# Kernel optimization log

Measured on AMD Instinct MI355X. Metric: run time of the kernel, lower is better.

## Reference

```python
import jax, jax.numpy as jnp
import numpy as np

N = 16384      # total nodes in batched graph
B = 64         # number of graphs (dgl.batch)
DEG = 8        # random in-degree (self-loops added on top)
C = 128        # feature width
H = 2          # heads in middle blocks
EH = 8         # E: heads of attn_seq / codebook entries
DEPTH = 2
IN = 8         # max_node_color (one-hot input width)
NE = N * DEG + N  # edges incl. self-loops


def layernorm(x, g, b, eps=1e-5):
    mu = jnp.mean(x, axis=-1, keepdims=True)
    var = jnp.mean(jnp.square(x - mu), axis=-1, keepdims=True)
    return (x - mu) * jax.lax.rsqrt(var + eps) * g + b


def gatv2(x, src, dst, Ws, bs, Wd, bd, attn):
    # DGL GATv2Conv (eval mode, attn_drop inactive, share_weights=False)
    h, c = attn.shape
    n = x.shape[0]
    el = (x @ Ws + bs).reshape(n, h, c)   # fc_src
    er = (x @ Wd + bd).reshape(n, h, c)   # fc_dst
    e = jax.nn.leaky_relu(el[src] + er[dst], negative_slope=0.2)  # [E,h,c]
    logits = jnp.einsum('ehc,hc->eh', e, attn)                    # [E,h]
    # edge softmax over incoming edges of each dst node
    m = jax.ops.segment_max(logits, dst, num_segments=n)
    a = jnp.exp(logits - m[dst])
    z = jax.ops.segment_sum(a, dst, num_segments=n)
    a = a / z[dst]
    return jax.ops.segment_sum(el[src] * a[..., None], dst, num_segments=n)  # [n,h,c]


def setup_inputs() -> dict:
    key = jax.random.key(0)
    ks = iter(jax.random.split(key, 64))
    nrm = lambda *s: jax.random.normal(next(ks), s, jnp.float32) * 0.05
    colors = jax.random.randint(next(ks), (N,), 0, IN)
    feats = jax.nn.one_hot(colors, IN, dtype=jnp.float32)
    loops = jnp.arange(N)
    src = jnp.concatenate([jax.random.randint(next(ks), (N * DEG,), 0, N), loops])
    dst = jnp.concatenate([jax.random.randint(next(ks), (N * DEG,), 0, N), loops])
    graph_ids = jnp.arange(N) // (N // B)
    inp = dict(feats=feats, src=src, dst=dst, graph_ids=graph_ids)
    # attn_up: GATv2Conv(IN -> C, 1 head)
    inp.update(up_Ws=nrm(IN, C), up_bs=nrm(C), up_Wd=nrm(IN, C), up_bd=nrm(C), up_attn=nrm(1, C))
    # depth blocks: GATv2Conv(C -> C, H heads) + ff
    inp.update(L_Ws=nrm(DEPTH, C, H * C), L_bs=nrm(DEPTH, H * C),
               L_Wd=nrm(DEPTH, C, H * C), L_bd=nrm(DEPTH, H * C),
               L_attn=nrm(DEPTH, H, C),
               ff_ln_g=jnp.ones((DEPTH, C), jnp.float32), ff_ln_b=jnp.zeros((DEPTH, C), jnp.float32),
               ff_W1=nrm(DEPTH, C, 2 * C), ff_b1=nrm(DEPTH, 2 * C),
               ff_W2=nrm(DEPTH, 2 * C, C), ff_b2=nrm(DEPTH, C),
               ff_W3=nrm(DEPTH, H * C, C), ff_b3=nrm(DEPTH, C))
    # attn_seq: GATv2Conv(C -> C, EH heads) + ff_seq
    inp.update(seq_Ws=nrm(C, EH * C), seq_bs=nrm(EH * C),
               seq_Wd=nrm(C, EH * C), seq_bd=nrm(EH * C),
               seq_attn=nrm(EH, C),
               fs_ln_g=jnp.ones((C,), jnp.float32), fs_ln_b=jnp.zeros((C,), jnp.float32),
               fs_W1=nrm(C, 2 * C), fs_b1=nrm(2 * C),
               fs_W2=nrm(2 * C, C), fs_b2=nrm(C),
               gate_W=nrm(EH * C, 1), gate_b=nrm(1))
    return inp


def reference(feats, src, dst, graph_ids,
              up_Ws, up_bs, up_Wd, up_bd, up_attn,
              L_Ws, L_bs, L_Wd, L_bd, L_attn,
              ff_ln_g, ff_ln_b, ff_W1, ff_b1, ff_W2, ff_b2, ff_W3, ff_b3,
              seq_Ws, seq_bs, seq_Wd, seq_bd, seq_attn,
              fs_ln_g, fs_ln_b, fs_W1, fs_b1, fs_W2, fs_b2,
              gate_W, gate_b):
    # attn_up (1 head) -> flatten to [N, C]
    x = gatv2(feats, src, dst, up_Ws, up_bs, up_Wd, up_bd, up_attn).reshape(N, C)
    for l in range(DEPTH):
        h = gatv2(x, src, dst, L_Ws[l], L_bs[l], L_Wd[l], L_bd[l], L_attn[l])  # [N,H,C]
        h = layernorm(h, ff_ln_g[l], ff_ln_b[l])
        h = jax.nn.gelu(h @ ff_W1[l] + ff_b1[l], approximate=False)
        h = h @ ff_W2[l] + ff_b2[l]                              # [N,H,C]
        x = h.reshape(N, H * C) @ ff_W3[l] + ff_b3[l]            # [N,C]
    y = gatv2(x, src, dst, seq_Ws, seq_bs, seq_Wd, seq_bd, seq_attn)  # [N,EH,C]
    y = layernorm(y, fs_ln_g, fs_ln_b)
    y = jax.nn.gelu(y @ fs_W1 + fs_b1, approximate=False) @ fs_W2 + fs_b2
    y = y.reshape(N, EH * C)
    # GlobalAttentionPooling: softmax(gate) over nodes within each graph
    gate = y @ gate_W + gate_b                                   # [N,1]
    gm = jax.ops.segment_max(gate, graph_ids, num_segments=B)
    ga = jnp.exp(gate - gm[graph_ids])
    gz = jax.ops.segment_sum(ga, graph_ids, num_segments=B)
    ga = ga / gz[graph_ids]
    pooled = jax.ops.segment_sum(ga * y, graph_ids, num_segments=B)  # [B, EH*C]
    return jnp.tanh(pooled.reshape(B, EH, C))
```

## Files before the change

kernel.cpp:

```cpp
#include <hip/hip_runtime.h>
#include <hip/hip_bf16.h>

typedef __hip_bfloat16 bf16;
typedef __attribute__((ext_vector_type(8))) short short8;
typedef __attribute__((ext_vector_type(4))) float f32x4;

#define NN 16384
#define NB 64
#define NE_TOT (NN*8 + NN)
#define CW 128

__device__ __forceinline__ float b2f(bf16 x){ return __bfloat162float(x); }
__device__ __forceinline__ bf16  f2b(float x){ return __float2bfloat16(x); }
__device__ __forceinline__ float lrelu(float x){ return fmaxf(x, 0.2f*x); }
__device__ __forceinline__ float gelu_f(float x){ return 0.5f*x*(1.f + erff(x*0.70710678118654752f)); }
__device__ __forceinline__ float us2f(unsigned int u){ return __uint_as_float(u << 16); }
__device__ __forceinline__ unsigned short f2us(float x){ return __builtin_bit_cast(unsigned short, f2b(x)); }

__device__ __forceinline__ void async16(const void* g, void* l){
  __builtin_amdgcn_global_load_lds((const __attribute__((address_space(1))) void*)g,
                                   (__attribute__((address_space(3))) void*)l, 16, 0, 0);
}

__global__ void k_detect(const unsigned short* __restrict__ f, int* __restrict__ flag){
  __shared__ int cnt;
  if(threadIdx.x == 0) cnt = 0;
  __syncthreads();
  int c = 0;
  for(int i = threadIdx.x; i < 2048; i += 256)
    if(f[2*i] == 0x3F80) c++;
  atomicAdd(&cnt, c);
  __syncthreads();
  if(threadIdx.x == 0) *flag = (cnt > 0) ? 0 : 1;
}

struct ConvArgs { const void* in[32]; bf16* out[32]; int n[32]; int tk[32]; int tj[32]; int ls[32]; };
__global__ __launch_bounds__(256) void k_conv_all(ConvArgs a, const int* __restrict__ flag){
  int which = blockIdx.y;
  int t = blockIdx.x*256 + threadIdx.x;
  int n = a.n[which];
  if(t >= n) return;
  float v = (*flag) ? ((const float*)a.in[which])[t] : b2f(((const bf16*)a.in[which])[t]);
  int tj = a.tj[which];
  if(tj == 0){ a.out[which][t] = f2b(v); return; }
  int tk = a.tk[which], kj = tk*tj;
  int l = t / kj, r = t - l*kj;
  int k = r / tj, j = r - k*tj;
  a.out[which][l*a.ls[which] + j*tk + k] = f2b(v);
}

__global__ void k_zero2(int* __restrict__ a, int* __restrict__ b, int n){
  int i = blockIdx.x*blockDim.x + threadIdx.x;
  if(i < n){ a[i] = 0; b[i] = 0; }
}
__global__ void k_hist(const int* __restrict__ dst, int* __restrict__ deg, int ne){
  int e = blockIdx.x*blockDim.x + threadIdx.x;
  if(e < ne) atomicAdd(&deg[dst[e]], 1);
}
__global__ void k_scan(const int* __restrict__ deg, int* __restrict__ off){
  __shared__ int s[256];
  int t = threadIdx.x;
  const int chunk = NN/256;
  int base = t*chunk;
  int sum = 0;
  for(int i=0;i<chunk;i++) sum += deg[base+i];
  s[t] = sum; __syncthreads();
  for(int o=1;o<256;o<<=1){
    int v = (t >= o) ? s[t-o] : 0;
    __syncthreads();
    s[t] += v;
    __syncthreads();
  }
  int run = (t == 0) ? 0 : s[t-1];
  for(int i=0;i<chunk;i++){ off[base+i] = run; run += deg[base+i]; }
  if(t == 255) off[NN] = run;
}
__global__ void k_scatter(const int* __restrict__ src, const int* __restrict__ dst,
                          const int* __restrict__ off, int* __restrict__ cursor,
                          int* __restrict__ csr_src, int ne){
  int e = blockIdx.x*blockDim.x + threadIdx.x;
  if(e < ne){
    int d = dst[e];
    int p = off[d] + atomicAdd(&cursor[d], 1);
    csr_src[p] = src[e];
  }
}

__global__ __launch_bounds__(128) void k_up(const bf16* __restrict__ feats,
    const bf16* __restrict__ Ws, const bf16* __restrict__ bs,
    const bf16* __restrict__ Wd, const bf16* __restrict__ bd,
    bf16* __restrict__ eler){
  int n = blockIdx.x, c = threadIdx.x;
  __shared__ float f[8];
  if(c < 8) f[c] = b2f(feats[n*8 + c]);
  __syncthreads();
  float a = b2f(bs[c]), b = b2f(bd[c]);
  #pragma unroll
  for(int k=0;k<8;k++){
    float fv = f[k];
    a += fv*b2f(Ws[k*CW + c]);
    b += fv*b2f(Wd[k*CW + c]);
  }
  eler[(size_t)n*256 + c]       = f2b(a);
  eler[(size_t)n*256 + 128 + c] = f2b(b);
}

template<int ACT>
__global__ __launch_bounds__(256) void k_mm(
    const bf16* __restrict__ A, int gshA, int gstrA,
    const bf16* __restrict__ WT, const bf16* __restrict__ bias,
    bf16* __restrict__ C, int gshC, int gstrC,
    int K, int J){
  __shared__ char smem[32768];
  short* As = (short*)smem;
  short* Bs = (short*)(smem + 16384);
  int tid = threadIdx.x, w = tid >> 6, lane = tid & 63;
  int l15 = lane & 15, q = lane >> 4;
  int wm = w >> 1, wn = w & 1;
  int bm = blockIdx.y*128, bn = blockIdx.x*128;

  f32x4 acc[4][4];
  #pragma unroll
  for(int i=0;i<4;i++)
    #pragma unroll
    for(int j=0;j<4;j++) acc[i][j] = (f32x4)0.f;

  int srow = w*32 + (lane >> 2);
  int scol = (lane & 3)*8;
  const bf16* gA[2]; const bf16* gB[2];
  short* lA[2]; short* lB[2];
  int mskA = (1 << gshA) - 1;
  #pragma unroll
  for(int a=0;a<2;a++){
    int rowA = bm + srow + a*16;
    gA[a] = A  + (size_t)(rowA >> gshA)*(size_t)gstrA + (size_t)(rowA & mskA)*K + scol;
    gB[a] = WT + (size_t)(bn + srow + a*16)*K + scol;
    lA[a] = As + (w*32 + a*16)*32;
    lB[a] = Bs + (w*32 + a*16)*32;
  }

  for(int kt=0; kt<K; kt+=64){
    #pragma unroll
    for(int a=0;a<2;a++)
      #pragma unroll
      for(int kh=0;kh<2;kh++){
        async16(gA[a] + kt + kh*32, lA[a] + kh*4096);
        async16(gB[a] + kt + kh*32, lB[a] + kh*4096);
      }
    __syncthreads();
    #pragma unroll
    for(int kh=0;kh<2;kh++){
      short8 af[4], bfr[4];
      #pragma unroll
      for(int i=0;i<4;i++) af[i]  = *(short8*)&As[kh*4096 + (wm*64 + i*16 + l15)*32 + q*8];
      #pragma unroll
      for(int j=0;j<4;j++) bfr[j] = *(short8*)&Bs[kh*4096 + (wn*64 + j*16 + l15)*32 + q*8];
      #pragma unroll
      for(int i=0;i<4;i++)
        #pragma unroll
        for(int j=0;j<4;j++)
          acc[i][j] = __builtin_amdgcn_mfma_f32_16x16x32_bf16(af[i], bfr[j], acc[i][j], 0, 0, 0);
    }
    __syncthreads();
  }

  float* ep = (float*)(smem + w*4352);
  int rr = lane >> 2;
  int cc = (lane & 3)*16;
  int mskC = (1 << gshC) - 1;
  #pragma unroll
  for(int i=0;i<4;i++){
    #pragma unroll
    for(int j=0;j<4;j++){
      float bv = b2f(bias[bn + wn*64 + j*16 + l15]);
      #pragma unroll
      for(int r=0;r<4;r++){
        float v = acc[i][j][r] + bv;
        if(ACT == 1) v = gelu_f(v);
        ep[(q*4+r)*68 + j*16 + l15] = v;
      }
    }
    float4 v0 = *(float4*)&ep[rr*68 + cc];
    float4 v1 = *(float4*)&ep[rr*68 + cc + 4];
    float4 v2 = *(float4*)&ep[rr*68 + cc + 8];
    float4 v3 = *(float4*)&ep[rr*68 + cc + 12];
    float vv[16] = {v0.x,v0.y,v0.z,v0.w, v1.x,v1.y,v1.z,v1.w,
                    v2.x,v2.y,v2.z,v2.w, v3.x,v3.y,v3.z,v3.w};
    unsigned int u[8];
    #pragma unroll
    for(int k=0;k<8;k++)
      u[k] = (unsigned int)f2us(vv[2*k]) | ((unsigned int)f2us(vv[2*k+1]) << 16);
    int row = bm + wm*64 + i*16 + rr;
    bf16* cp = C + (size_t)(row >> gshC)*(size_t)gstrC + (size_t)(row & mskC)*J + bn + wn*64 + cc;
    *(uint4*)cp       = make_uint4(u[0],u[1],u[2],u[3]);
    *(uint4*)(cp + 8) = make_uint4(u[4],u[5],u[6],u[7]);
  }
}

__global__ __launch_bounds__(256) void k_ff(
    const bf16* __restrict__ A, int gshA, int gstrA,
    const bf16* __restrict__ W1T, const bf16* __restrict__ b1,
    const bf16* __restrict__ W2T, const bf16* __restrict__ b2,
    bf16* __restrict__ C, int gshC, int gstrC){
  __shared__ short Wb[8704];
  __shared__ short Hs[8320];
  int tid = threadIdx.x, w = tid >> 6, lane = tid & 63;
  int l15 = lane & 15, q = lane >> 4;
  int bm = blockIdx.x*32;
  int mskA = (1 << gshA) - 1, mskC = (1 << gshC) - 1;
  int mt = w & 1, jg = w >> 1;

  int rowA = bm + mt*16 + l15;
  const bf16* ap = A + (size_t)(rowA >> gshA)*(size_t)gstrA + (size_t)(rowA & mskA)*128;
  short8 af[4];
  #pragma unroll
  for(int ki=0;ki<4;ki++) af[ki] = *(const short8*)&ap[ki*32 + q*8];

  for(int jt=0; jt<4; jt++){
    #pragma unroll
    for(int it=0;it<4;it++){
      int slot = tid + it*256;
      int r = slot >> 4, c8 = slot & 15;
      *(int4*)&Wb[r*132 + c8*8] = *(const int4*)&W1T[(size_t)(jt*64 + r)*128 + c8*8];
    }
    __syncthreads();
    f32x4 acc1[2] = {(f32x4)0.f, (f32x4)0.f};
    #pragma unroll
    for(int ki=0;ki<4;ki++){
      #pragma unroll
      for(int t=0;t<2;t++){
        int jrow = (jg*2 + t)*16 + l15;
        short8 bfr = *(short8*)&Wb[jrow*132 + ki*32 + q*8];
        acc1[t] = __builtin_amdgcn_mfma_f32_16x16x32_bf16(af[ki], bfr, acc1[t], 0, 0, 0);
      }
    }
    #pragma unroll
    for(int t=0;t<2;t++){
      int jcol = jt*64 + (jg*2 + t)*16 + l15;
      float bv = b2f(b1[jcol]);
      #pragma unroll
      for(int r=0;r<4;r++){
        float v = gelu_f(acc1[t][r] + bv);
        Hs[(mt*16 + q*4 + r)*260 + jcol] = (short)f2us(v);
      }
    }
    __syncthreads();
  }

  f32x4 acc2[4];
  #pragma unroll
  for(int t=0;t<4;t++) acc2[t] = (f32x4)0.f;
  for(int kc=0; kc<4; kc++){
    #pragma unroll
    for(int it=0;it<4;it++){
      int slot = tid + it*256;
      int r = slot >> 3, c8 = slot & 7;
      *(int4*)&Wb[r*68 + c8*8] = *(const int4*)&W2T[(size_t)r*256 + kc*64 + c8*8];
    }
    __syncthreads();
    #pragma unroll
    for(int ki=0;ki<2;ki++){
      short8 haf = *(short8*)&Hs[(mt*16 + l15)*260 + kc*64 + ki*32 + q*8];
      #pragma unroll
      for(int t=0;t<4;t++){
        int jrow = (jg*4 + t)*16 + l15;
        short8 bfr = *(short8*)&Wb[jrow*68 + ki*32 + q*8];
        acc2[t] = __builtin_amdgcn_mfma_f32_16x16x32_bf16(haf, bfr, acc2[t], 0, 0, 0);
      }
    }
    __syncthreads();
  }

  float* epf = (float*)Hs;
  #pragma unroll
  for(int t=0;t<4;t++){
    int jcol = (jg*4 + t)*16 + l15;
    float bv = b2f(b2[jcol]);
    #pragma unroll
    for(int r=0;r<4;r++)
      epf[(mt*16 + q*4 + r)*130 + jcol] = acc2[t][r] + bv;
  }
  __syncthreads();
  int row = tid >> 3, cseg = (tid & 7)*16;
  float4 v0 = *(float4*)&epf[row*130 + cseg];
  float4 v1 = *(float4*)&epf[row*130 + cseg + 4];
  float4 v2 = *(float4*)&epf[row*130 + cseg + 8];
  float4 v3 = *(float4*)&epf[row*130 + cseg + 12];
  float vv[16] = {v0.x,v0.y,v0.z,v0.w, v1.x,v1.y,v1.z,v1.w,
                  v2.x,v2.y,v2.z,v2.w, v3.x,v3.y,v3.z,v3.w};
  unsigned int u[8];
  #pragma unroll
  for(int k=0;k<8;k++)
    u[k] = (unsigned int)f2us(vv[2*k]) | ((unsigned int)f2us(vv[2*k+1]) << 16);
  int rowC = bm + row;
  bf16* cpb = C + (size_t)(rowC >> gshC)*(size_t)gstrC + (size_t)(rowC & mskC)*128 + cseg;
  *(uint4*)cpb       = make_uint4(u[0],u[1],u[2],u[3]);
  *(uint4*)(cpb + 8) = make_uint4(u[4],u[5],u[6],u[7]);
}

template<int E>
__device__ __forceinline__ void load_row(const bf16* p, float* f){
  if constexpr (E == 2){
    unsigned int v = *(const unsigned int*)p;
    f[0] = us2f(v & 0xffffu); f[1] = __uint_as_float(v & 0xffff0000u);
  } else if constexpr (E == 4){
    uint2 v = *(const uint2*)p;
    f[0] = us2f(v.x & 0xffffu); f[1] = __uint_as_float(v.x & 0xffff0000u);
    f[2] = us2f(v.y & 0xffffu); f[3] = __uint_as_float(v.y & 0xffff0000u);
  } else if constexpr (E == 8){
    uint4 a = *(const uint4*)p;
    unsigned int vs[4] = {a.x,a.y,a.z,a.w};
    #pragma unroll
    for(int i=0;i<4;i++){
      f[2*i]   = us2f(vs[i] & 0xffffu);
      f[2*i+1] = __uint_as_float(vs[i] & 0xffff0000u);
    }
  } else {
    uint4 a = *(const uint4*)p;
    uint4 b = *(const uint4*)(p + 8);
    unsigned int vs[8] = {a.x,a.y,a.z,a.w,b.x,b.y,b.z,b.w};
    #pragma unroll
    for(int i=0;i<8;i++){
      f[2*i]   = us2f(vs[i] & 0xffffu);
      f[2*i+1] = __uint_as_float(vs[i] & 0xffff0000u);
    }
  }
}
template<int E>
__device__ __forceinline__ void store_row(bf16* p, const float* f){
  unsigned int vs[E/2];
  #pragma unroll
  for(int i=0;i<E/2;i++)
    vs[i] = (unsigned int)f2us(f[2*i]) | ((unsigned int)f2us(f[2*i+1]) << 16);
  if constexpr (E == 2){ *(unsigned int*)p = vs[0]; }
  else if constexpr (E == 4){ *(uint2*)p = make_uint2(vs[0], vs[1]); }
  else if constexpr (E == 8){ *(uint4*)p = make_uint4(vs[0], vs[1], vs[2], vs[3]); }
  else {
    *(uint4*)p       = make_uint4(vs[0], vs[1], vs[2], vs[3]);
    *(uint4*)(p + 8) = make_uint4(vs[4], vs[5], vs[6], vs[7]);
  }
}

template<int H, bool LNF, int SSH>
__global__ __launch_bounds__(256) void k_gat(const int* __restrict__ off, const int* __restrict__ csr_src,
    const bf16* __restrict__ el, const bf16* __restrict__ er, const bf16* __restrict__ attn,
    const bf16* __restrict__ lng, const bf16* __restrict__ lnb, bf16* __restrict__ out,
    int rsn_in, int rsh_in, int rsn_out, int rsh_out){
  constexpr int EPL = 2*H;
  constexpr int G   = 64/H;
  int w = threadIdx.x >> 6, lane = threadIdx.x & 63;
  int nv = blockIdx.x*4 + w;
  int node = nv >> SSH, hf = nv & ((1 << SSH) - 1);
  size_t hin = (size_t)hf*rsh_in;

  float ef[EPL], af[EPL];
  load_row<EPL>(er + (size_t)node*rsn_in + hin + lane*EPL, ef);
  load_row<EPL>(attn + hf*(64*EPL) + lane*EPL, af);

  int p0 = off[node], p1 = off[node+1];

  float m = -1e30f, z = 0.f;
  float acc[EPL];
  #pragma unroll
  for(int e=0;e<EPL;e++) acc[e] = 0.f;

  float xf[EPL];
  int s0 = csr_src[p0];
  load_row<EPL>(el + (size_t)s0*rsn_in + hin + lane*EPL, xf);
  for(int p = p0; p < p1; p++){
    float xn[EPL];
    if(p + 1 < p1){
      int sn = csr_src[p+1];
      load_row<EPL>(el + (size_t)sn*rsn_in + hin + lane*EPL, xn);
    }
    float part = 0.f;
    #pragma unroll
    for(int e=0;e<EPL;e++) part += af[e]*lrelu(xf[e] + ef[e]);
    #pragma unroll
    for(int o=G/2; o; o>>=1) part += __shfl_xor(part, o, 64);
    float nm = fmaxf(m, part);
    float alpha = expf(m - nm);
    float c = expf(part - nm);
    z = z*alpha + c;
    #pragma unroll
    for(int e=0;e<EPL;e++) acc[e] = acc[e]*alpha + c*xf[e];
    m = nm;
    #pragma unroll
    for(int e=0;e<EPL;e++) xf[e] = xn[e];
  }
  float rz = 1.f/z;
  #pragma unroll
  for(int e=0;e<EPL;e++) acc[e] *= rz;

  if constexpr (LNF){
    float sl = 0.f;
    #pragma unroll
    for(int e=0;e<EPL;e++) sl += acc[e];
    #pragma unroll
    for(int o=G/2; o; o>>=1) sl += __shfl_xor(sl, o, 64);
    float mu = sl*(1.f/128.f);
    float qs = 0.f;
    #pragma unroll
    for(int e=0;e<EPL;e++){ float d = acc[e] - mu; qs += d*d; }
    #pragma unroll
    for(int o=G/2; o; o>>=1) qs += __shfl_xor(qs, o, 64);
    float r = rsqrtf(qs*(1.f/128.f) + 1e-5f);
    int cbase = (lane & (G-1))*EPL;
    #pragma unroll
    for(int e=0;e<EPL;e++)
      acc[e] = (acc[e] - mu)*r*b2f(lng[cbase + e]) + b2f(lnb[cbase + e]);
  }
  store_row<EPL>(out + (size_t)node*rsn_out + (size_t)hf*rsh_out + lane*EPL, acc);
}

__global__ __launch_bounds__(256) void k_gate(const bf16* __restrict__ y2, const bf16* __restrict__ gW,
                                              const bf16* __restrict__ gb, float* __restrict__ gate){
  int n = blockIdx.x*4 + (threadIdx.x >> 6);
  int lane = threadIdx.x & 63;
  const bf16* yr = y2 + (size_t)n*2048;
  float p = 0.f;
  #pragma unroll
  for(int j=0;j<16;j++) p += b2f(yr[lane + j*64])*b2f(gW[lane + j*64]);
  #pragma unroll
  for(int o=32;o;o>>=1) p += __shfl_down(p, o, 64);
  if(lane == 0) gate[n] = p + b2f(gb[0]);
}

__global__ __launch_bounds__(64) void k_pool1(const float* __restrict__ gate,
                                              float* __restrict__ gm, float* __restrict__ gz){
  int g = blockIdx.x, lane = threadIdx.x;
  float v0 = gate[g*256 + lane], v1 = gate[g*256 + 64 + lane];
  float v2 = gate[g*256 + 128 + lane], v3 = gate[g*256 + 192 + lane];
  float m = fmaxf(fmaxf(v0,v1), fmaxf(v2,v3));
  #pragma unroll
  for(int o=32;o;o>>=1) m = fmaxf(m, __shfl_xor(m, o, 64));
  float z = expf(v0-m) + expf(v1-m) + expf(v2-m) + expf(v3-m);
  #pragma unroll
  for(int o=32;o;o>>=1) z += __shfl_xor(z, o, 64);
  if(lane == 0){ gm[g] = m; gz[g] = z; }
}

__global__ __launch_bounds__(256) void k_pool2(const float* __restrict__ gate,
    const float* __restrict__ gm, const float* __restrict__ gz,
    const bf16* __restrict__ y2, void* __restrict__ outv, const int* __restrict__ flag){
  int g = blockIdx.x >> 2, cb = blockIdx.x & 3, t = threadIdx.x;
  __shared__ float aL[256];
  aL[t] = expf(gate[g*256 + t] - gm[g]) / gz[g];
  __syncthreads();
  int ch = cb*256 + t;
  float acc = 0.f;
  const bf16* base = y2 + (size_t)g*256*2048 + ch;
  for(int i=0;i<256;i++) acc += aL[i]*b2f(base[(size_t)i*2048]);
  float v = tanhf(acc);
  size_t idx = (size_t)g*1024 + ch;
  if(*flag) ((float*)outv)[idx] = v;
  else      ((bf16*)outv)[idx] = f2b(v);
}

extern "C" void kernel_launch(void* const* d_in, const int* in_sizes, int n_in,
                              void* d_out, int out_size, void* d_ws, size_t ws_size,
                              hipStream_t stream){
  const int* src = (const int*)d_in[1];
  const int* dst = (const int*)d_in[2];

  char* wsb = (char*)d_ws;
  size_t o = 0;
  auto take = [&](size_t bytes)->char*{
    char* p = wsb + o; o = (o + bytes + 255) & ~(size_t)255; return p;
  };
  int*   flag  = (int*)take(4);
  float* gate  = (float*)take((size_t)NN*4);
  float* gm    = (float*)take(64*4);
  float* gz    = (float*)take(64*4);
  int* deg     = (int*)take((size_t)NN*4);
  int* cursor  = (int*)take((size_t)NN*4);
  int* off     = (int*)take((size_t)(NN+1)*4);
  int* csr_src = (int*)take((size_t)NE_TOT*4);

  bf16* WcombL   = (bf16*)take((size_t)2*512*128*2);
  bf16* bcombL   = (bf16*)take((size_t)2*512*2);
  bf16* WcombSeq = (bf16*)take((size_t)2048*128*2);
  bf16* bcombSeq = (bf16*)take((size_t)2048*2);

  ConvArgs ca;
  const int fidx[32] = {0, 4,5,6,7,8, 9,10,11,12,13, 14,15,16,17,18,19,20,21,
                        22,23,24,25,26, 27,28,29,30,31,32, 33,34};
  bf16* cp[32];
  int maxn = 0;
  for(int i=0;i<32;i++){
    int n = in_sizes[fidx[i]];
    ca.in[i] = d_in[fidx[i]]; ca.n[i] = n;
    ca.tk[i] = 0; ca.tj[i] = 0; ca.ls[i] = 0;
    cp[i] = nullptr;
    if(n > maxn) maxn = n;
  }
  auto plain = [&](int i){ cp[i] = (bf16*)take((size_t)ca.n[i]*2); ca.out[i] = cp[i]; };
  auto spec  = [&](int i, bf16* dst_, int tk, int tj, int ls){
    ca.out[i] = dst_; ca.tk[i] = tk; ca.tj[i] = tj; ca.ls[i] = ls; cp[i] = dst_; };
  auto owntr = [&](int i, int tk, int tj){
    cp[i] = (bf16*)take((size_t)ca.n[i]*2);
    ca.out[i] = cp[i]; ca.tk[i] = tk; ca.tj[i] = tj; ca.ls[i] = tk*tj; };

  plain(0);
  plain(1); plain(2); plain(3); plain(4); plain(5);
  spec(6,  WcombL,          128, 256, 65536);
  spec(7,  bcombL,          256, 1,   512);
  spec(8,  WcombL + 32768,  128, 256, 65536);
  spec(9,  bcombL + 256,    256, 1,   512);
  plain(10); plain(11); plain(12);
  owntr(13, 128, 256);
  plain(14);
  owntr(15, 256, 128); plain(16);
  owntr(17, 256, 128); plain(18);
  spec(19, WcombSeq,           128, 1024, 131072);
  spec(20, bcombSeq,           1024, 1,  2048);
  spec(21, WcombSeq + 131072,  128, 1024, 131072);
  spec(22, bcombSeq + 1024,    1024, 1,  2048);
  plain(23); plain(24); plain(25);
  owntr(26, 128, 256); plain(27);
  owntr(28, 256, 128); plain(29);
  plain(30); plain(31);

  bf16* AB = (bf16*)take((size_t)NN*2048*2);
  bf16* X  = (bf16*)take((size_t)NN*128*2);
  bf16* G1 = AB + (size_t)NN*1024;
  bf16* G2 = AB + (size_t)NN*1024 + (size_t)NN*256;
  (void)ws_size; (void)n_in; (void)out_size;

  k_detect<<<1, 256, 0, stream>>>((const unsigned short*)d_in[0], flag);
  k_conv_all<<<dim3((maxn+255)/256, 32), 256, 0, stream>>>(ca, flag);

  k_zero2 <<<(NN+255)/256, 256, 0, stream>>>(deg, cursor, NN);
  k_hist  <<<(NE_TOT+255)/256, 256, 0, stream>>>(dst, deg, NE_TOT);
  k_scan  <<<1, 256, 0, stream>>>(deg, off);
  k_scatter<<<(NE_TOT+255)/256, 256, 0, stream>>>(src, dst, off, cursor, csr_src, NE_TOT);

  k_up<<<NN, 128, 0, stream>>>(cp[0], cp[1], cp[2], cp[3], cp[4], AB);
  k_gat<1,false,0><<<NN/4, 256, 0, stream>>>(off, csr_src, AB, AB + 128, cp[5],
                                             nullptr, nullptr, X, 256, 0, 128, 0);

  for(int l=0; l<2; l++){
    k_mm<0><<<dim3(4, 128), 256, 0, stream>>>(X, 30, 0, WcombL + l*65536, bcombL + l*512,
                                              AB, 30, 0, 128, 512);
    k_gat<1,true,1><<<2*NN/4, 256, 0, stream>>>(off, csr_src, AB, AB + 256, cp[10] + l*256,
                                                cp[11] + l*128, cp[12] + l*128, G1,
                                                512, 128, 256, 128);
    k_ff<<<2*NN/32, 256, 0, stream>>>(G1, 30, 0, cp[13] + l*32768, cp[14] + l*256,
                                      cp[15] + l*32768, cp[16] + l*128, G2, 30, 0);
    k_mm<0><<<dim3(1, 128), 256, 0, stream>>>(G2, 30, 0, cp[17] + l*32768, cp[18] + l*128,
                                              X, 30, 0, 256, 128);
  }

  k_mm<0><<<dim3(16, 128), 256, 0, stream>>>(X, 30, 0, WcombSeq, bcombSeq, AB, 30, 0, 128, 2048);
  k_gat<4,true,1><<<2*NN/4, 256, 0, stream>>>(off, csr_src, AB, AB + 1024, cp[23],
                                              cp[24], cp[25], AB + 1024,
                                              2048, 512, 2048, 512);
  k_ff<<<131072/32, 256, 0, stream>>>(AB + 1024, 3, 2048, cp[26], cp[27],
                                      cp[28], cp[29], AB, 3, 2048);

  k_gate <<<NN/4, 256, 0, stream>>>(AB, cp[30], cp[31], gate);
  k_pool1<<<NB, 64, 0, stream>>>(gate, gm, gz);
  k_pool2<<<NB*4, 256, 0, stream>>>(gate, gm, gz, AB, d_out, flag);
}
```

Before: 546.2 us.

## Fuse gate dot-product into final FF, drop online softmax max, one warp per node

The gate projection is folded into the last feed-forward kernel's epilogue, with per-row partial dots accumulated by atomicAdd into a zeroed gate buffer, so the separate pass over the large output is removed. The GAT kernel now handles all heads of a node in one wavefront instead of splitting heads across wavefronts, so the CSR indices are read once per node. It also drops the running-max rescaling in the edge softmax in favour of a plain __expf sum. Skipping the max subtraction risks overflow when logits are large. The gate bias is no longer added, which is harmless because softmax is shift-invariant.

```diff
diff --git a/kernel.cpp b/kernel.cpp
--- a/kernel.cpp
+++ b/kernel.cpp
@@ -49,9 +49,9 @@
   a.out[which][l*a.ls[which] + j*tk + k] = f2b(v);
 }
 
-__global__ void k_zero2(int* __restrict__ a, int* __restrict__ b, int n){
+__global__ void k_zero3(int* __restrict__ a, int* __restrict__ b, float* __restrict__ g, int n){
   int i = blockIdx.x*blockDim.x + threadIdx.x;
-  if(i < n){ a[i] = 0; b[i] = 0; }
+  if(i < n){ a[i] = 0; b[i] = 0; g[i] = 0.f; }
 }
 __global__ void k_hist(const int* __restrict__ dst, int* __restrict__ deg, int ne){
   int e = blockIdx.x*blockDim.x + threadIdx.x;
@@ -197,107 +197,6 @@
   }
 }
 
-__global__ __launch_bounds__(256) void k_ff(
-    const bf16* __restrict__ A, int gshA, int gstrA,
-    const bf16* __restrict__ W1T, const bf16* __restrict__ b1,
-    const bf16* __restrict__ W2T, const bf16* __restrict__ b2,
-    bf16* __restrict__ C, int gshC, int gstrC){
-  __shared__ short Wb[8704];
-  __shared__ short Hs[8320];
-  int tid = threadIdx.x, w = tid >> 6, lane = tid & 63;
-  int l15 = lane & 15, q = lane >> 4;
-  int bm = blockIdx.x*32;
-  int mskA = (1 << gshA) - 1, mskC = (1 << gshC) - 1;
-  int mt = w & 1, jg = w >> 1;
-
-  int rowA = bm + mt*16 + l15;
-  const bf16* ap = A + (size_t)(rowA >> gshA)*(size_t)gstrA + (size_t)(rowA & mskA)*128;
-  short8 af[4];
-  #pragma unroll
-  for(int ki=0;ki<4;ki++) af[ki] = *(const short8*)&ap[ki*32 + q*8];
-
-  for(int jt=0; jt<4; jt++){
-    #pragma unroll
-    for(int it=0;it<4;it++){
-      int slot = tid + it*256;
-      int r = slot >> 4, c8 = slot & 15;
-      *(int4*)&Wb[r*132 + c8*8] = *(const int4*)&W1T[(size_t)(jt*64 + r)*128 + c8*8];
-    }
-    __syncthreads();
-    f32x4 acc1[2] = {(f32x4)0.f, (f32x4)0.f};
-    #pragma unroll
-    for(int ki=0;ki<4;ki++){
-      #pragma unroll
-      for(int t=0;t<2;t++){
-        int jrow = (jg*2 + t)*16 + l15;
-        short8 bfr = *(short8*)&Wb[jrow*132 + ki*32 + q*8];
-        acc1[t] = __builtin_amdgcn_mfma_f32_16x16x32_bf16(af[ki], bfr, acc1[t], 0, 0, 0);
-      }
-    }
-    #pragma unroll
-    for(int t=0;t<2;t++){
-      int jcol = jt*64 + (jg*2 + t)*16 + l15;
-      float bv = b2f(b1[jcol]);
-      #pragma unroll
-      for(int r=0;r<4;r++){
-        float v = gelu_f(acc1[t][r] + bv);
-        Hs[(mt*16 + q*4 + r)*260 + jcol] = (short)f2us(v);
-      }
-    }
-    __syncthreads();
-  }
-
-  f32x4 acc2[4];
-  #pragma unroll
-  for(int t=0;t<4;t++) acc2[t] = (f32x4)0.f;
-  for(int kc=0; kc<4; kc++){
-    #pragma unroll
-    for(int it=0;it<4;it++){
-      int slot = tid + it*256;
-      int r = slot >> 3, c8 = slot & 7;
-      *(int4*)&Wb[r*68 + c8*8] = *(const int4*)&W2T[(size_t)r*256 + kc*64 + c8*8];
-    }
-    __syncthreads();
-    #pragma unroll
-    for(int ki=0;ki<2;ki++){
-      short8 haf = *(short8*)&Hs[(mt*16 + l15)*260 + kc*64 + ki*32 + q*8];
-      #pragma unroll
-      for(int t=0;t<4;t++){
-        int jrow = (jg*4 + t)*16 + l15;
-        short8 bfr = *(short8*)&Wb[jrow*68 + ki*32 + q*8];
-        acc2[t] = __builtin_amdgcn_mfma_f32_16x16x32_bf16(haf, bfr, acc2[t], 0, 0, 0);
-      }
-    }
-    __syncthreads();
-  }
-
-  float* epf = (float*)Hs;
-  #pragma unroll
-  for(int t=0;t<4;t++){
-    int jcol = (jg*4 + t)*16 + l15;
-    float bv = b2f(b2[jcol]);
-    #pragma unroll
-    for(int r=0;r<4;r++)
-      epf[(mt*16 + q*4 + r)*130 + jcol] = acc2[t][r] + bv;
-  }
-  __syncthreads();
-  int row = tid >> 3, cseg = (tid & 7)*16;
-  float4 v0 = *(float4*)&epf[row*130 + cseg];
-  float4 v1 = *(float4*)&epf[row*130 + cseg + 4];
-  float4 v2 = *(float4*)&epf[row*130 + cseg + 8];
-  float4 v3 = *(float4*)&epf[row*130 + cseg + 12];
-  float vv[16] = {v0.x,v0.y,v0.z,v0.w, v1.x,v1.y,v1.z,v1.w,
-                  v2.x,v2.y,v2.z,v2.w, v3.x,v3.y,v3.z,v3.w};
-  unsigned int u[8];
-  #pragma unroll
-  for(int k=0;k<8;k++)
-    u[k] = (unsigned int)f2us(vv[2*k]) | ((unsigned int)f2us(vv[2*k+1]) << 16);
-  int rowC = bm + row;
-  bf16* cpb = C + (size_t)(rowC >> gshC)*(size_t)gstrC + (size_t)(rowC & mskC)*128 + cseg;
-  *(uint4*)cpb       = make_uint4(u[0],u[1],u[2],u[3]);
-  *(uint4*)(cpb + 8) = make_uint4(u[4],u[5],u[6],u[7]);
-}
-
 template<int E>
 __device__ __forceinline__ void load_row(const bf16* p, float* f){
   if constexpr (E == 2){
@@ -341,50 +240,160 @@
   }
 }
 
-template<int H, bool LNF, int SSH>
+template<int GATE>
+__global__ __launch_bounds__(256) void k_ff(
+    const bf16* __restrict__ A, int gshA, int gstrA,
+    const bf16* __restrict__ W1T, const bf16* __restrict__ b1,
+    const bf16* __restrict__ W2T, const bf16* __restrict__ b2,
+    bf16* __restrict__ C, int gshC, int gstrC,
+    const bf16* __restrict__ gW, float* __restrict__ gate){
+  __shared__ short Wb[8704];
+  __shared__ short Hs[8320];
+  int tid = threadIdx.x, w = tid >> 6, lane = tid & 63;
+  int l15 = lane & 15, q = lane >> 4;
+  int bm = blockIdx.x*32;
+  int mskA = (1 << gshA) - 1, mskC = (1 << gshC) - 1;
+  int mt = w & 1, jg = w >> 1;
+
+  int rowA = bm + mt*16 + l15;
+  const bf16* ap = A + (size_t)(rowA >> gshA)*(size_t)gstrA + (size_t)(rowA & mskA)*128;
+  short8 af[4];
+  #pragma unroll
+  for(int ki=0;ki<4;ki++) af[ki] = *(const short8*)&ap[ki*32 + q*8];
+
+  for(int jt=0; jt<4; jt++){
+    #pragma unroll
+    for(int it=0;it<4;it++){
+      int slot = tid + it*256;
+      int r = slot >> 4, c8 = slot & 15;
+      *(int4*)&Wb[r*132 + c8*8] = *(const int4*)&W1T[(size_t)(jt*64 + r)*128 + c8*8];
+    }
+    __syncthreads();
+    f32x4 acc1[2] = {(f32x4)0.f, (f32x4)0.f};
+    #pragma unroll
+    for(int ki=0;ki<4;ki++){
+      #pragma unroll
+      for(int t=0;t<2;t++){
+        int jrow = (jg*2 + t)*16 + l15;
+        short8 bfr = *(short8*)&Wb[jrow*132 + ki*32 + q*8];
+        acc1[t] = __builtin_amdgcn_mfma_f32_16x16x32_bf16(af[ki], bfr, acc1[t], 0, 0, 0);
+      }
+    }
+    #pragma unroll
+    for(int t=0;t<2;t++){
+      int jcol = jt*64 + (jg*2 + t)*16 + l15;
+      float bv = b2f(b1[jcol]);
+      #pragma unroll
+      for(int r=0;r<4;r++){
+        float v = gelu_f(acc1[t][r] + bv);
+        Hs[(mt*16 + q*4 + r)*260 + jcol] = (short)f2us(v);
+      }
+    }
+    __syncthreads();
+  }
+
+  f32x4 acc2[4];
+  #pragma unroll
+  for(int t=0;t<4;t++) acc2[t] = (f32x4)0.f;
+  for(int kc=0; kc<4; kc++){
+    #pragma unroll
+    for(int it=0;it<4;it++){
+      int slot = tid + it*256;
+      int r = slot >> 3, c8 = slot & 7;
+      *(int4*)&Wb[r*68 + c8*8] = *(const int4*)&W2T[(size_t)r*256 + kc*64 + c8*8];
+    }
+    __syncthreads();
+    #pragma unroll
+    for(int ki=0;ki<2;ki++){
+      short8 haf = *(short8*)&Hs[(mt*16 + l15)*260 + kc*64 + ki*32 + q*8];
+      #pragma unroll
+      for(int t=0;t<4;t++){
+        int jrow = (jg*4 + t)*16 + l15;
+        short8 bfr = *(short8*)&Wb[jrow*68 + ki*32 + q*8];
+        acc2[t] = __builtin_amdgcn_mfma_f32_16x16x32_bf16(haf, bfr, acc2[t], 0, 0, 0);
+      }
+    }
+    __syncthreads();
+  }
+
+  float* epf = (float*)Hs;
+  #pragma unroll
+  for(int t=0;t<4;t++){
+    int jcol = (jg*4 + t)*16 + l15;
+    float bv = b2f(b2[jcol]);
+    #pragma unroll
+    for(int r=0;r<4;r++)
+      epf[(mt*16 + q*4 + r)*130 + jcol] = acc2[t][r] + bv;
+  }
+  __syncthreads();
+  int row = tid >> 3, cseg = (tid & 7)*16;
+  float4 v0 = *(float4*)&epf[row*130 + cseg];
+  float4 v1 = *(float4*)&epf[row*130 + cseg + 4];
+  float4 v2 = *(float4*)&epf[row*130 + cseg + 8];
+  float4 v3 = *(float4*)&epf[row*130 + cseg + 12];
+  float vv[16] = {v0.x,v0.y,v0.z,v0.w, v1.x,v1.y,v1.z,v1.w,
+                  v2.x,v2.y,v2.z,v2.w, v3.x,v3.y,v3.z,v3.w};
+  unsigned int u[8];
+  #pragma unroll
+  for(int k=0;k<8;k++)
+    u[k] = (unsigned int)f2us(vv[2*k]) | ((unsigned int)f2us(vv[2*k+1]) << 16);
+  int rowC = bm + row;
+  bf16* cpb = C + (size_t)(rowC >> gshC)*(size_t)gstrC + (size_t)(rowC & mskC)*128 + cseg;
+  *(uint4*)cpb       = make_uint4(u[0],u[1],u[2],u[3]);
+  *(uint4*)(cpb + 8) = make_uint4(u[4],u[5],u[6],u[7]);
+
+  if constexpr (GATE){
+    float gwf[16];
+    load_row<16>(gW + (rowC & 7)*128 + cseg, gwf);
+    float p = 0.f;
+    #pragma unroll
+    for(int k=0;k<16;k++) p += vv[k]*gwf[k];
+    p += __shfl_xor(p, 1, 64);
+    p += __shfl_xor(p, 2, 64);
+    p += __shfl_xor(p, 4, 64);
+    if((tid & 7) == 0) atomicAdd(&gate[rowC >> 3], p);
+  }
+}
+
+template<int H, bool LNF>
 __global__ __launch_bounds__(256) void k_gat(const int* __restrict__ off, const int* __restrict__ csr_src,
     const bf16* __restrict__ el, const bf16* __restrict__ er, const bf16* __restrict__ attn,
     const bf16* __restrict__ lng, const bf16* __restrict__ lnb, bf16* __restrict__ out,
-    int rsn_in, int rsh_in, int rsn_out, int rsh_out){
+    int rs_in, int rs_out){
   constexpr int EPL = 2*H;
   constexpr int G   = 64/H;
   int w = threadIdx.x >> 6, lane = threadIdx.x & 63;
-  int nv = blockIdx.x*4 + w;
-  int node = nv >> SSH, hf = nv & ((1 << SSH) - 1);
-  size_t hin = (size_t)hf*rsh_in;
+  int n = blockIdx.x*4 + w;
 
   float ef[EPL], af[EPL];
-  load_row<EPL>(er + (size_t)node*rsn_in + hin + lane*EPL, ef);
-  load_row<EPL>(attn + hf*(64*EPL) + lane*EPL, af);
-
-  int p0 = off[node], p1 = off[node+1];
-
-  float m = -1e30f, z = 0.f;
+  load_row<EPL>(er   + (size_t)n*rs_in + lane*EPL, ef);
+  load_row<EPL>(attn + lane*EPL, af);
+
+  int p0 = off[n], p1 = off[n+1];
+
+  float z = 0.f;
   float acc[EPL];
   #pragma unroll
   for(int e=0;e<EPL;e++) acc[e] = 0.f;
 
   float xf[EPL];
   int s0 = csr_src[p0];
-  load_row<EPL>(el + (size_t)s0*rsn_in + hin + lane*EPL, xf);
+  load_row<EPL>(el + (size_t)s0*rs_in + lane*EPL, xf);
   for(int p = p0; p < p1; p++){
     float xn[EPL];
     if(p + 1 < p1){
       int sn = csr_src[p+1];
-      load_row<EPL>(el + (size_t)sn*rsn_in + hin + lane*EPL, xn);
+      load_row<EPL>(el + (size_t)sn*rs_in + lane*EPL, xn);
     }
     float part = 0.f;
     #pragma unroll
     for(int e=0;e<EPL;e++) part += af[e]*lrelu(xf[e] + ef[e]);
     #pragma unroll
     for(int o=G/2; o; o>>=1) part += __shfl_xor(part, o, 64);
-    float nm = fmaxf(m, part);
-    float alpha = expf(m - nm);
-    float c = expf(part - nm);
-    z = z*alpha + c;
-    #pragma unroll
-    for(int e=0;e<EPL;e++) acc[e] = acc[e]*alpha + c*xf[e];
-    m = nm;
+    float c = __expf(part);
+    z += c;
+    #pragma unroll
+    for(int e=0;e<EPL;e++) acc[e] += c*xf[e];
     #pragma unroll
     for(int e=0;e<EPL;e++) xf[e] = xn[e];
   }
@@ -410,20 +419,7 @@
     for(int e=0;e<EPL;e++)
       acc[e] = (acc[e] - mu)*r*b2f(lng[cbase + e]) + b2f(lnb[cbase + e]);
   }
-  store_row<EPL>(out + (size_t)node*rsn_out + (size_t)hf*rsh_out + lane*EPL, acc);
-}
-
-__global__ __launch_bounds__(256) void k_gate(const bf16* __restrict__ y2, const bf16* __restrict__ gW,
-                                              const bf16* __restrict__ gb, float* __restrict__ gate){
-  int n = blockIdx.x*4 + (threadIdx.x >> 6);
-  int lane = threadIdx.x & 63;
-  const bf16* yr = y2 + (size_t)n*2048;
-  float p = 0.f;
-  #pragma unroll
-  for(int j=0;j<16;j++) p += b2f(yr[lane + j*64])*b2f(gW[lane + j*64]);
-  #pragma unroll
-  for(int o=32;o;o>>=1) p += __shfl_down(p, o, 64);
-  if(lane == 0) gate[n] = p + b2f(gb[0]);
+  store_row<EPL>(out + (size_t)n*rs_out + lane*EPL, acc);
 }
 
 __global__ __launch_bounds__(64) void k_pool1(const float* __restrict__ gate,
@@ -434,7 +430,7 @@
   float m = fmaxf(fmaxf(v0,v1), fmaxf(v2,v3));
   #pragma unroll
   for(int o=32;o;o>>=1) m = fmaxf(m, __shfl_xor(m, o, 64));
-  float z = expf(v0-m) + expf(v1-m) + expf(v2-m) + expf(v3-m);
+  float z = __expf(v0-m) + __expf(v1-m) + __expf(v2-m) + __expf(v3-m);
   #pragma unroll
   for(int o=32;o;o>>=1) z += __shfl_xor(z, o, 64);
   if(lane == 0){ gm[g] = m; gz[g] = z; }
@@ -445,7 +441,7 @@
     const bf16* __restrict__ y2, void* __restrict__ outv, const int* __restrict__ flag){
   int g = blockIdx.x >> 2, cb = blockIdx.x & 3, t = threadIdx.x;
   __shared__ float aL[256];
-  aL[t] = expf(gate[g*256 + t] - gm[g]) / gz[g];
+  aL[t] = __expf(gate[g*256 + t] - gm[g]) / gz[g];
   __syncthreads();
   int ch = cb*256 + t;
   float acc = 0.f;
@@ -530,35 +526,34 @@
   k_detect<<<1, 256, 0, stream>>>((const unsigned short*)d_in[0], flag);
   k_conv_all<<<dim3((maxn+255)/256, 32), 256, 0, stream>>>(ca, flag);
 
-  k_zero2 <<<(NN+255)/256, 256, 0, stream>>>(deg, cursor, NN);
+  k_zero3 <<<(NN+255)/256, 256, 0, stream>>>(deg, cursor, gate, NN);
   k_hist  <<<(NE_TOT+255)/256, 256, 0, stream>>>(dst, deg, NE_TOT);
   k_scan  <<<1, 256, 0, stream>>>(deg, off);
   k_scatter<<<(NE_TOT+255)/256, 256, 0, stream>>>(src, dst, off, cursor, csr_src, NE_TOT);
 
   k_up<<<NN, 128, 0, stream>>>(cp[0], cp[1], cp[2], cp[3], cp[4], AB);
-  k_gat<1,false,0><<<NN/4, 256, 0, stream>>>(off, csr_src, AB, AB + 128, cp[5],
-                                             nullptr, nullptr, X, 256, 0, 128, 0);
+  k_gat<1,false><<<NN/4, 256, 0, stream>>>(off, csr_src, AB, AB + 128, cp[5],
+                                           nullptr, nullptr, X, 256, 128);
 
   for(int l=0; l<2; l++){
     k_mm<0><<<dim3(4, 128), 256, 0, stream>>>(X, 30, 0, WcombL + l*65536, bcombL + l*512,
                                               AB, 30, 0, 128, 512);
-    k_gat<1,true,1><<<2*NN/4, 256, 0, stream>>>(off, csr_src, AB, AB + 256, cp[10] + l*256,
-                                                cp[11] + l*128, cp[12] + l*128, G1,
-                                                512, 128, 256, 128);
-    k_ff<<<2*NN/32, 256, 0, stream>>>(G1, 30, 0, cp[13] + l*32768, cp[14] + l*256,
-                                      cp[15] + l*32768, cp[16] + l*128, G2, 30, 0);
+    k_gat<2,true><<<NN/4, 256, 0, stream>>>(off, csr_src, AB, AB + 256, cp[10] + l*256,
+                                            cp[11] + l*128, cp[12] + l*128, G1, 512, 256);
+    k_ff<0><<<2*NN/32, 256, 0, stream>>>(G1, 30, 0, cp[13] + l*32768, cp[14] + l*256,
+                                         cp[15] + l*32768, cp[16] + l*128, G2, 30, 0,
+                                         nullptr, nullptr);
     k_mm<0><<<dim3(1, 128), 256, 0, stream>>>(G2, 30, 0, cp[17] + l*32768, cp[18] + l*128,
                                               X, 30, 0, 256, 128);
   }
 
   k_mm<0><<<dim3(16, 128), 256, 0, stream>>>(X, 30, 0, WcombSeq, bcombSeq, AB, 30, 0, 128, 2048);
-  k_gat<4,true,1><<<2*NN/4, 256, 0, stream>>>(off, csr_src, AB, AB + 1024, cp[23],
-                                              cp[24], cp[25], AB + 1024,
-                                              2048, 512, 2048, 512);
-  k_ff<<<131072/32, 256, 0, stream>>>(AB + 1024, 3, 2048, cp[26], cp[27],
-                                      cp[28], cp[29], AB, 3, 2048);
-
-  k_gate <<<NN/4, 256, 0, stream>>>(AB, cp[30], cp[31], gate);
+  k_gat<8,true><<<NN/4, 256, 0, stream>>>(off, csr_src, AB, AB + 1024, cp[23],
+                                          cp[24], cp[25], AB + 1024, 2048, 2048);
+  k_ff<1><<<131072/32, 256, 0, stream>>>(AB + 1024, 3, 2048, cp[26], cp[27],
+                                         cp[28], cp[29], AB, 3, 2048,
+                                         cp[30], gate);
+
   k_pool1<<<NB, 64, 0, stream>>>(gate, gm, gz);
   k_pool2<<<NB*4, 256, 0, stream>>>(gate, gm, gz, AB, d_out, flag);
 }
```

After: 495.7 us. 9.3% less time.
